# Kernel optimization log

Measured on AMD Instinct MI355X. Metric: run time of the kernel, lower is better.

## Reference

```python
import jax, jax.numpy as jnp
import numpy as np

# Multi-scale AvgPool3d pyramid (stride 1, zero padding, count_include_pad=True as in torch)
KERNELS = [(1, 1, 1), (1, 5, 5), (3, 13, 13), (5, 23, 23), (7, 31, 31), (9, 41, 41)]
WEIGHTS = [w / 100.0 for w in [20, 20, 20, 20, 20, 20, 10, 10]]
EPS = 1e-7  # BatchDiceLoss epsilon


def avgpool3d(x, k):
    # x: [B, C, D, H, W]; separable sum-pool per axis then divide by full kernel size
    # (equivalent to torch AvgPool3d with count_include_pad=True, stride 1, pad=(k-1)//2)
    y = x
    for axis, ks in zip((2, 3, 4), k):
        if ks > 1:
            window = [1] * 5
            window[axis] = ks
            pad = [(0, 0)] * 5
            pad[axis] = (ks // 2, ks // 2)
            y = jax.lax.reduce_window(y, 0.0, jax.lax.add, tuple(window), (1,) * 5, tuple(pad))
    return y / float(np.prod(k))


def batch_dice(pred, target):
    # BatchDiceLoss([1.0]): single label channel 0, flattened over the whole batch
    p = pred[:, 0].reshape(-1)
    t = target[:, 0].reshape(-1)
    inter = jnp.sum(p * t)
    return 1.0 - (2.0 * inter) / (jnp.sum(p) + jnp.sum(t) + EPS)


def multi_scale_dc(pred, target):
    loss = 0.0
    for k in KERNELS:
        pp = avgpool3d(avgpool3d(pred, k), k)   # pool applied twice per scale
        tt = avgpool3d(avgpool3d(target, k), k)
        loss = loss + batch_dice(pp, tt)
    return loss / len(KERNELS)


def setup_inputs() -> dict:
    key = jax.random.key(0)
    ks = jax.random.split(key, 14)
    vol = (4, 1, 28, 160, 160)
    u = lambda k: jax.random.uniform(k, vol, dtype=jnp.float32)
    return {
        "pr_core_c": u(ks[0]),
        "pr_core_p": u(ks[1]),
        "gt_core": u(ks[2]),
        "pr_lesion_c": u(ks[3]),
        "pr_lesion_p": u(ks[4]),
        "gt_lesion": u(ks[5]),
        "pr_penu_c": u(ks[6]),
        "pr_penu_p": u(ks[7]),
        "gt_penu": u(ks[8]),
        "output": jax.random.uniform(ks[9], (4, 6, 28, 160, 160), dtype=jnp.float32),
        "off_core_c": jax.random.normal(ks[10], (4, 3), dtype=jnp.float32),
        "off_penu_p": jax.random.normal(ks[11], (4, 3), dtype=jnp.float32),
        "off_target_c": jax.random.normal(ks[12], (4, 3), dtype=jnp.float32),
        "off_target_p": jax.random.normal(ks[13], (4, 3), dtype=jnp.float32),
    }


def reference(pr_core_c, pr_core_p, gt_core, pr_lesion_c, pr_lesion_p, gt_lesion,
              pr_penu_c, pr_penu_p, gt_penu, output,
              off_core_c, off_penu_p, off_target_c, off_target_p):
    loss = WEIGHTS[0] * multi_scale_dc(pr_core_c, gt_core)
    loss += WEIGHTS[1] * multi_scale_dc(pr_core_p, gt_core)
    loss += WEIGHTS[2] * multi_scale_dc(pr_lesion_c, gt_lesion)
    loss += WEIGHTS[3] * multi_scale_dc(pr_lesion_p, gt_lesion)
    loss += WEIGHTS[4] * multi_scale_dc(pr_penu_c, gt_penu)
    loss += WEIGHTS[5] * multi_scale_dc(pr_penu_p, gt_penu)
    # temporal monotonicity penalty: mean(|diff| - diff) per consecutive time pair
    diff = output[:, 1:] - output[:, :-1]           # [B, T-1, D, H, W]
    loss += WEIGHTS[6] * jnp.sum(jnp.mean(jnp.abs(diff) - diff, axis=(0, 2, 3, 4)))
    loss += WEIGHTS[7] * jnp.mean(jnp.abs(off_core_c - off_target_c))
    loss += WEIGHTS[7] * jnp.mean(jnp.abs(off_penu_p - off_target_p))
    return loss
```

## Files before the change

kernel.cpp:

```cpp
#include <hip/hip_runtime.h>
#include <hip/hip_fp16.h>


#define DIMB 4
#define DIMD 28
#define DIMH 160
#define DIMW 160
#define HW   (DIMH * DIMW)
#define DHW  (DIMD * HW)
#define VOL_N (DIMB * DHW)
#define DW   (DIMD * DIMW)
#define PGRID 640
#define NSLOTS 91
#define DICE_EPS 1e-7
#define TBL_OFF (480 * 1024)

__device__ __forceinline__ float u2f(int pos, int k, int L) {
    if (k == 1) return 1.f;
    int r = k >> 1;
    float s = 0.f;
    for (int j = max(pos - r, 0); j <= min(pos + r, L - 1); ++j)
        s += (float)(min(j + r, L - 1) - max(j - r, 0) + 1);
    return s / (float)(k * k);
}

__device__ __forceinline__ float wave_sum(float v) {
#pragma unroll
    for (int o = 1; o < 64; o <<= 1) v += __shfl_xor(v, o, 64);
    return v;
}

__device__ __forceinline__ __half2 shfl_h2(__half2 v, int src) {
    int x = __shfl(*reinterpret_cast<int*>(&v), src, 64);
    return *reinterpret_cast<__half2*>(&x);
}

template<int K>
__device__ __forceinline__ void hstore(const float (&raw)[40],
                                       unsigned char* __restrict__ ob,
                                       int l, int c, int wl, int h0)
{
    constexpr int R = K / 2;
    constexpr float INVK = 1.f / (float)K;
    float ox[40];
#pragma unroll
    for (int i = 0; i < 40; ++i) ox[i] = raw[i];
#pragma unroll
    for (int pass = 0; pass < 4; ++pass) {
        float lo[R], hi[R];
#pragma unroll
        for (int i = 0; i < R; ++i) {
            float a = __shfl(ox[40 - R + i], l - 16, 64);
            lo[i] = (c == 0) ? 0.f : a;
            float b = __shfl(ox[i], l + 16, 64);
            hi[i] = (c == 3) ? 0.f : b;
        }
#define HWIN(j) ((j) < R ? lo[(j)] : ((j) < R + 40 ? ox[(j) - R] : hi[(j) - R - 40]))
        float out[40];
        float s = 0.f;
#pragma unroll
        for (int j = 0; j <= 2 * R; ++j) s += HWIN(j);
        out[0] = s * INVK;
#pragma unroll
        for (int i = 1; i < 40; ++i) {
            s += HWIN(i + 2 * R) - HWIN(i - 1);
            out[i] = s * INVK;
        }
#undef HWIN
#pragma unroll
        for (int i = 0; i < 40; ++i) ox[i] = out[i];
    }
#pragma unroll
    for (int i = 0; i < 40; ++i)
        ob[(h0 + i) * DW + wl] = (unsigned char)__float2uint_rn(ox[i] * 255.f);
}

__global__ __launch_bounds__(256) void hpool_tbl(const float* __restrict__ g0,
    const float* __restrict__ g1, const float* __restrict__ g2,
    unsigned char* __restrict__ bufs, float* __restrict__ tbl)
{
    int bx = blockIdx.x;
    int t = threadIdx.x;
    if (bx < 840) {
        int u = bx * 2 + (t >> 7);
        int tt = t & 127;
        int g = u / 560, r = u - g * 560;
        int bd = r / 5, wt = r - bd * 5;
        int b = bd / DIMD, d = bd - b * DIMD;
        const float* in = (g == 0) ? g0 : (g == 1) ? g1 : g2;
        int l = tt & 63, v = tt >> 6;
        int c = l >> 4, wl = v * 16 + (l & 15), h0 = c * 40;
        const float* base = in + (size_t)bd * HW + wt * 32;
        float raw[40];
#pragma unroll
        for (int i = 0; i < 40; ++i) raw[i] = base[(h0 + i) * DIMW + wl];
        unsigned char* ob = bufs + (size_t)(g * 5) * VOL_N + (size_t)b * DHW
                          + d * DIMW + wt * 32;
        hstore<5> (raw, ob + 0 * (size_t)VOL_N, l, c, wl, h0);
        hstore<13>(raw, ob + 1 * (size_t)VOL_N, l, c, wl, h0);
        hstore<23>(raw, ob + 2 * (size_t)VOL_N, l, c, wl, h0);
        hstore<31>(raw, ob + 3 * (size_t)VOL_N, l, c, wl, h0);
        hstore<41>(raw, ob + 4 * (size_t)VOL_N, l, c, wl, h0);
    } else {
        const int KDa[6] = {1, 1, 3, 5, 7, 9};
        const int KHa[6] = {1, 5, 13, 23, 31, 41};
        for (int e = t; e < 1128; e += 256) {
            if (e < 960) tbl[e] = u2f(e % 160, KHa[e / 160], DIMH);
            else {
                int q = e - 960;
                tbl[e] = u2f(q % 28, KDa[q / 28], DIMD);
            }
        }
    }
}

template<int K, int KD>
__device__ __forceinline__ void wd_scale_pk(const unsigned char* __restrict__ tbA,
    const float4* __restrict__ c4, const float4* __restrict__ p4, int base4,
    unsigned int (*S)[164], float (*redS)[4], int t, int l, int wid, int rr,
    int c, bool act, double* __restrict__ partials, int slot_c, int slot_p,
    int bhA)
{
    constexpr int R = K / 2;
    const __half2 INVK2 = __float2half2_rn(1.f / (float)K);
    const __half2 Z2 = __float2half2_rn(0.f);
    __half2 ox[20];
    if (act) {
        unsigned int uA[5], uB[5];
#pragma unroll
        for (int q = 0; q < 5; ++q) {
            uA[q] = *(const unsigned int*)(tbA + 4 * q);
            uB[q] = *(const unsigned int*)(tbA + DW + 4 * q);
        }
#pragma unroll
        for (int q = 0; q < 5; ++q) {
#pragma unroll
            for (int j = 0; j < 4; ++j) {
                float fA = (float)((uA[q] >> (8 * j)) & 0xFFu);
                float fB = (float)((uB[q] >> (8 * j)) & 0xFFu);
                ox[4 * q + j] = __floats2half2_rn(fA, fB);
            }
        }
    } else {
#pragma unroll
        for (int i = 0; i < 20; ++i) ox[i] = Z2;
    }
#pragma unroll
    for (int pass = 0; pass < 4; ++pass) {
        __half2 lo[R], hi[R];
#pragma unroll
        for (int i = 0; i < R; ++i) {
            __half2 a = shfl_h2(ox[20 - R + i], l - 1);
            lo[i] = (c == 0) ? Z2 : a;
            __half2 b = shfl_h2(ox[i], l + 1);
            hi[i] = (c == 7) ? Z2 : b;
        }
#define WWIN(j) ((j) < R ? lo[(j)] : ((j) < R + 20 ? ox[(j) - R] : hi[(j) - R - 20]))
        __half2 out[20];
        __half2 s = Z2;
#pragma unroll
        for (int j = 0; j <= 2 * R; ++j) s = __hadd2(s, WWIN(j));
        out[0] = __hmul2(s, INVK2);
#pragma unroll
        for (int i = 1; i < 20; ++i) {
            s = __hadd2(s, __hsub2(WWIN(i + 2 * R), WWIN(i - 1)));
            out[i] = __hmul2(s, INVK2);
        }
#undef WWIN
#pragma unroll
        for (int i = 0; i < 20; ++i) ox[i] = out[i];
    }
    if (act) {
#pragma unroll
        for (int i = 0; i < 20; ++i)
            S[rr][c * 20 + i] = *reinterpret_cast<unsigned int*>(&ox[i]);
    }
    __syncthreads();
    if constexpr (KD > 1) {
        constexpr int RD = KD / 2;
        const __half2 INVKD2 = __float2half2_rn(1.f / (float)KD);
        if (t < DIMW) {
            __half2 x[28];
#pragma unroll
            for (int j = 0; j < 28; ++j)
                x[j] = *reinterpret_cast<const __half2*>(&S[j][t]);
#pragma unroll
            for (int p = 0; p < 4; ++p) {
                __half2 y[28];
                __half2 s = Z2;
#pragma unroll
                for (int j = 0; j <= RD; ++j) s = __hadd2(s, x[j]);
                y[0] = s;
#pragma unroll
                for (int i = 1; i < 28; ++i) {
                    if (i + RD < 28) s = __hadd2(s, x[i + RD]);
                    if (i - RD - 1 >= 0) s = __hsub2(s, x[i - RD - 1]);
                    y[i] = s;
                }
#pragma unroll
                for (int i = 0; i < 28; ++i) x[i] = __hmul2(y[i], INVKD2);
            }
#pragma unroll
            for (int j = 0; j < 28; ++j)
                S[j][t] = *reinterpret_cast<unsigned int*>(&x[j]);
        }
        __syncthreads();
    }
    float aicA = 0.f, aipA = 0.f, aicB = 0.f, aipB = 0.f;
    for (int e4 = t; e4 < 1120; e4 += 256) {
        int dd = e4 / 40, w4 = e4 - dd * 40;
        int fi = base4 + dd * (HW / 4) + w4;
        float4 vcA = c4[fi],      vpA = p4[fi];
        float4 vcB = c4[fi + 40], vpB = p4[fi + 40];
        const uint4 sv = *(const uint4*)&S[dd][4 * w4];
        float2 s0 = __half22float2(*reinterpret_cast<const __half2*>(&sv.x));
        float2 s1 = __half22float2(*reinterpret_cast<const __half2*>(&sv.y));
        float2 s2 = __half22float2(*reinterpret_cast<const __half2*>(&sv.z));
        float2 s3 = __half22float2(*reinterpret_cast<const __half2*>(&sv.w));
        aicA += vcA.x*s0.x + vcA.y*s1.x + vcA.z*s2.x + vcA.w*s3.x;
        aipA += vpA.x*s0.x + vpA.y*s1.x + vpA.z*s2.x + vpA.w*s3.x;
        aicB += vcB.x*s0.y + vcB.y*s1.y + vcB.z*s2.y + vcB.w*s3.y;
        aipB += vpB.x*s0.y + vpB.y*s1.y + vpB.z*s2.y + vpB.w*s3.y;
    }
    const float SC = 1.f / 255.f;
    float v0 = wave_sum(aicA) * SC, v1 = wave_sum(aipA) * SC;
    float v2 = wave_sum(aicB) * SC, v3 = wave_sum(aipB) * SC;
    if (l == 0) {
        redS[wid][0] = v0; redS[wid][1] = v1;
        redS[wid][2] = v2; redS[wid][3] = v3;
    }
    __syncthreads();
    if (t < 4) {
        double rv = (double)redS[0][t] + redS[1][t] + redS[2][t] + redS[3][t];
        int slot = (t & 1) ? slot_p : slot_c;
        int bh = bhA + (t >> 1);
        partials[(size_t)slot * PGRID + bh] = rv;
    }
}

__global__ __launch_bounds__(256) void wd_mix(const unsigned char* __restrict__ bufs,
    const float* __restrict__ pc0, const float* __restrict__ pp0,
    const float* __restrict__ pc1, const float* __restrict__ pp1,
    const float* __restrict__ pc2, const float* __restrict__ pp2,
    const float* __restrict__ tr0, const float* __restrict__ tr1,
    const float* __restrict__ tr2, const float* __restrict__ o6,
    const float* __restrict__ tbl, double* __restrict__ partials)
{
    __shared__ __align__(16) unsigned int S[DIMD][164];
    __shared__ float redS[4][24];
    int bx0 = blockIdx.x;
    int t = threadIdx.x;

    if (bx0 < 1920) {
        int g = bx0 / PGRID, blk = bx0 - g * PGRID;
        const float* pc = (g == 0) ? pc0 : (g == 1) ? pc1 : pc2;
        const float* pp = (g == 0) ? pp0 : (g == 1) ? pp1 : pp2;
        const float* tr = (g == 0) ? tr0 : (g == 1) ? tr1 : tr2;
        const float4* c4p = (const float4*)pc;
        const float4* p4p = (const float4*)pp;
        const float4* t4p = (const float4*)tr;
        float vals[20];
#pragma unroll
        for (int i = 0; i < 20; ++i) vals[i] = 0.f;
        const int N4 = VOL_N / 4;
        for (int i4 = blk * 256 + t; i4 < N4; i4 += PGRID * 256) {
            int w4 = i4 % 40;
            int rest = i4 / 40;
            int h = rest % DIMH;
            int d = (rest / DIMH) % DIMD;
            float4 vc = c4p[i4], vp = p4p[i4], vt = t4p[i4];
            vals[0] += vc.x*vt.x + vc.y*vt.y + vc.z*vt.z + vc.w*vt.w;
            vals[1] += vp.x*vt.x + vp.y*vt.y + vp.z*vt.z + vp.w*vt.w;
#pragma unroll
            for (int s = 0; s < 6; ++s) {
                float cdh = tbl[960 + s * 28 + d] * tbl[s * 160 + h];
                const float4 cw = *(const float4*)(tbl + s * 160 + 4 * w4);
                vals[2 + s]  += cdh * (cw.x*vc.x + cw.y*vc.y + cw.z*vc.z + cw.w*vc.w);
                vals[8 + s]  += cdh * (cw.x*vp.x + cw.y*vp.y + cw.z*vp.z + cw.w*vp.w);
                vals[14 + s] += cdh * (cw.x*vt.x + cw.y*vt.y + cw.z*vt.z + cw.w*vt.w);
            }
        }
        int lane = t & 63, wid = t >> 6;
#pragma unroll
        for (int i = 0; i < 20; ++i) {
            float rv = wave_sum(vals[i]);
            if (lane == 0) redS[wid][i] = rv;
        }
        __syncthreads();
        if (t < 20) {
            double rv = (double)redS[0][t] + redS[1][t] + redS[2][t] + redS[3][t];
            int slot;
            if (t == 0) slot = (2 * g) * 6;
            else if (t == 1) slot = (2 * g + 1) * 6;
            else {
                int i = t - 2, vv = i / 6, s = i % 6;
                slot = (vv == 0) ? 36 + (2 * g) * 6 + s
                     : (vv == 1) ? 36 + (2 * g + 1) * 6 + s
                                 : 72 + g * 6 + s;
            }
            partials[(size_t)slot * PGRID + blk] = rv;
        }
        return;
    }

    if (bx0 < 2560) {
        int mb = bx0 - 1920;
        const int N4 = VOL_N / 4, PB = N4 / DIMB;
        float acc = 0.f;
        const float4* p = (const float4*)o6;
        for (int i = mb * 256 + t; i < N4; i += PGRID * 256) {
            int b = i / PB, r4 = i - b * PB;
            size_t a = (size_t)(b * 6) * PB + r4;
            float4 prev = p[a];
#pragma unroll
            for (int cc = 1; cc < 6; ++cc) {
                float4 cur = p[a + (size_t)cc * PB];
                acc += fmaxf(prev.x - cur.x, 0.f) + fmaxf(prev.y - cur.y, 0.f)
                     + fmaxf(prev.z - cur.z, 0.f) + fmaxf(prev.w - cur.w, 0.f);
                prev = cur;
            }
        }
        float rv = wave_sum(acc * 2.f);
        int lane = t & 63, wid = t >> 6;
        if (lane == 0) redS[wid][0] = rv;
        __syncthreads();
        if (t == 0)
            partials[(size_t)90 * PGRID + mb] =
                (double)redS[0][0] + redS[1][0] + redS[2][0] + redS[3][0];
        return;
    }

    int bxs = bx0 - 2560;
    int w = (bxs & 7) * 600 + (bxs >> 3);
    int u = w / 5, q = w - u * 5;
    int g = u / 320, pj = u - g * 320;
    int bhA = 2 * pj;
    int b = bhA / DIMH, h = bhA - b * DIMH;
    const float* pc = (g == 0) ? pc0 : (g == 1) ? pc1 : pc2;
    const float* pp = (g == 0) ? pp0 : (g == 1) ? pp1 : pp2;
    int base4 = b * (DHW / 4) + h * 40;
    const float4* c4 = (const float4*)pc;
    const float4* p4 = (const float4*)pp;
    int l = t & 63, wid = t >> 6;
    int rr = wid * 7 + (l >> 3), c = l & 7;
    bool act = (l < 56);
    int sbuf = 4 - q;
    const unsigned char* tbA = bufs + (size_t)(g * 5 + sbuf) * VOL_N
                             + (size_t)b * DHW + (size_t)h * DW
                             + rr * DIMW + c * 20;
    int s = 5 - q;
    int slot_c = (2 * g) * 6 + s, slot_p = (2 * g + 1) * 6 + s;
    switch (q) {
        case 0: wd_scale_pk<41, 9>(tbA, c4, p4, base4, S, (float(*)[4])&redS[0][0], t, l, wid, rr, c, act, partials, slot_c, slot_p, bhA); break;
        case 1: wd_scale_pk<31, 7>(tbA, c4, p4, base4, S, (float(*)[4])&redS[0][0], t, l, wid, rr, c, act, partials, slot_c, slot_p, bhA); break;
        case 2: wd_scale_pk<23, 5>(tbA, c4, p4, base4, S, (float(*)[4])&redS[0][0], t, l, wid, rr, c, act, partials, slot_c, slot_p, bhA); break;
        case 3: wd_scale_pk<13, 3>(tbA, c4, p4, base4, S, (float(*)[4])&redS[0][0], t, l, wid, rr, c, act, partials, slot_c, slot_p, bhA); break;
        default: wd_scale_pk<5, 1>(tbA, c4, p4, base4, S, (float(*)[4])&redS[0][0], t, l, wid, rr, c, act, partials, slot_c, slot_p, bhA); break;
    }
}

__global__ __launch_bounds__(64) void fin_pre(const double* __restrict__ partials,
                                              double* __restrict__ ssum)
{
    int slot = blockIdx.x, t = threadIdx.x;
    double a = 0.0;
    for (int i = t; i < PGRID; i += 64) a += partials[(size_t)slot * PGRID + i];
#pragma unroll
    for (int o = 1; o < 64; o <<= 1) a += __shfl_xor(a, o, 64);
    if (t == 0) ssum[slot] = a;
}

__global__ void finalize(const double* __restrict__ ssum,
                         const float* __restrict__ off_a,
                         const float* __restrict__ off_b,
                         const float* __restrict__ off_ta,
                         const float* __restrict__ off_tb,
                         float* __restrict__ out)
{
    if (threadIdx.x == 0) {
        double loss = 0.0;
        for (int pair = 0; pair < 6; ++pair) {
            for (int s = 0; s < 6; ++s) {
                double inter = ssum[pair * 6 + s];
                double sp = ssum[36 + pair * 6 + s];
                double st = ssum[72 + (pair / 2) * 6 + s];
                loss += 0.2 * (1.0 - 2.0 * inter / (sp + st + DICE_EPS)) / 6.0;
            }
        }
        loss += 0.1 * (ssum[90] / (double)VOL_N);
        double oa = 0.0, ob = 0.0;
        for (int i = 0; i < 12; ++i) {
            oa += fabs((double)off_a[i] - (double)off_ta[i]);
            ob += fabs((double)off_b[i] - (double)off_tb[i]);
        }
        loss += 0.1 * (oa / 12.0) + 0.1 * (ob / 12.0);
        out[0] = (float)loss;
    }
}

extern "C" void kernel_launch(void* const* d_in, const int* in_sizes, int n_in,
                              void* d_out, int out_size, void* d_ws, size_t ws_size,
                              hipStream_t stream)
{
    double* partials = (double*)d_ws;
    double* ssum = partials + (size_t)NSLOTS * PGRID;
    float* tbl = (float*)((char*)d_ws + TBL_OFF);
    unsigned char* bufs = (unsigned char*)d_ws + 512 * 1024;

    const float* pred[6] = {(const float*)d_in[0], (const float*)d_in[1],
                            (const float*)d_in[3], (const float*)d_in[4],
                            (const float*)d_in[6], (const float*)d_in[7]};
    const float* gt[3] = {(const float*)d_in[2], (const float*)d_in[5],
                          (const float*)d_in[8]};

    hpool_tbl<<<841, 256, 0, stream>>>(gt[0], gt[1], gt[2], bufs, tbl);
    wd_mix<<<7360, 256, 0, stream>>>(bufs, pred[0], pred[1], pred[2], pred[3],
                                     pred[4], pred[5], gt[0], gt[1], gt[2],
                                     (const float*)d_in[9], tbl, partials);
    fin_pre<<<NSLOTS, 64, 0, stream>>>(partials, ssum);
    finalize<<<1, 64, 0, stream>>>(ssum,
                                   (const float*)d_in[10], (const float*)d_in[11],
                                   (const float*)d_in[12], (const float*)d_in[13],
                                   (float*)d_out);
}
```

Measured before the change: 120.0 us.

## Interleave block roles across grid and hoist loop-invariant W weights

```diff
diff --git a/kernel.cpp b/kernel.cpp
--- a/kernel.cpp
+++ b/kernel.cpp
@@ -250,21 +250,28 @@
     __shared__ float redS[4][24];
     int bx0 = blockIdx.x;
     int t = threadIdx.x;
-
-    if (bx0 < 1920) {
-        int g = bx0 / PGRID, blk = bx0 - g * PGRID;
+    int grp = bx0 / 23, pos = bx0 - grp * 23;
+
+    if (pos < 6) {
+        int did = grp * 6 + pos;
+        int g = did / PGRID, blk = did - g * PGRID;
         const float* pc = (g == 0) ? pc0 : (g == 1) ? pc1 : pc2;
         const float* pp = (g == 0) ? pp0 : (g == 1) ? pp1 : pp2;
         const float* tr = (g == 0) ? tr0 : (g == 1) ? tr1 : tr2;
         const float4* c4p = (const float4*)pc;
         const float4* p4p = (const float4*)pp;
         const float4* t4p = (const float4*)tr;
+        const int N4 = VOL_N / 4;
+        int i0 = blk * 256 + t;
+        int w4 = i0 % 40;
+        float4 cw4[6];
+#pragma unroll
+        for (int s = 0; s < 6; ++s)
+            cw4[s] = *(const float4*)(tbl + s * 160 + 4 * w4);
         float vals[20];
 #pragma unroll
         for (int i = 0; i < 20; ++i) vals[i] = 0.f;
-        const int N4 = VOL_N / 4;
-        for (int i4 = blk * 256 + t; i4 < N4; i4 += PGRID * 256) {
-            int w4 = i4 % 40;
+        for (int i4 = i0; i4 < N4; i4 += PGRID * 256) {
             int rest = i4 / 40;
             int h = rest % DIMH;
             int d = (rest / DIMH) % DIMD;
@@ -274,10 +281,9 @@
 #pragma unroll
             for (int s = 0; s < 6; ++s) {
                 float cdh = tbl[960 + s * 28 + d] * tbl[s * 160 + h];
-                const float4 cw = *(const float4*)(tbl + s * 160 + 4 * w4);
-                vals[2 + s]  += cdh * (cw.x*vc.x + cw.y*vc.y + cw.z*vc.z + cw.w*vc.w);
-                vals[8 + s]  += cdh * (cw.x*vp.x + cw.y*vp.y + cw.z*vp.z + cw.w*vp.w);
-                vals[14 + s] += cdh * (cw.x*vt.x + cw.y*vt.y + cw.z*vt.z + cw.w*vt.w);
+                vals[2 + s]  += cdh * (cw4[s].x*vc.x + cw4[s].y*vc.y + cw4[s].z*vc.z + cw4[s].w*vc.w);
+                vals[8 + s]  += cdh * (cw4[s].x*vp.x + cw4[s].y*vp.y + cw4[s].z*vp.z + cw4[s].w*vp.w);
+                vals[14 + s] += cdh * (cw4[s].x*vt.x + cw4[s].y*vt.y + cw4[s].z*vt.z + cw4[s].w*vt.w);
             }
         }
         int lane = t & 63, wid = t >> 6;
@@ -303,8 +309,8 @@
         return;
     }
 
-    if (bx0 < 2560) {
-        int mb = bx0 - 1920;
+    if (pos < 8) {
+        int mb = grp * 2 + (pos - 6);
         const int N4 = VOL_N / 4, PB = N4 / DIMB;
         float acc = 0.f;
         const float4* p = (const float4*)o6;
@@ -330,9 +336,8 @@
         return;
     }
 
-    int bxs = bx0 - 2560;
-    int w = (bxs & 7) * 600 + (bxs >> 3);
-    int u = w / 5, q = w - u * 5;
+    int sid = grp * 15 + (pos - 8);
+    int u = sid / 5, q = sid - u * 5;
     int g = u / 320, pj = u - g * 320;
     int bhA = 2 * pj;
     int b = bhA / DIMH, h = bhA - b * DIMH;
```

Result: slower. 125.6 us (+4.7%).
